# Performance work log

Measured on AMD Instinct MI355X. Metric: run time of the kernel, lower is better.

## Reference

```python
import jax, jax.numpy as jnp
import numpy as np

# static config (Phi-3-like with GQA)
B, S, H, HKV, D, BS = 2, 2048, 32, 8, 128, 64
HID = H * D
NB = B * (S // BS)  # total cache blocks
THETA = 10000.0


def rotate_half(x):
    x1, x2 = jnp.split(x, 2, axis=-1)
    return jnp.concatenate([-x2, x1], axis=-1)


def rope_cos_sin(positions):
    # positions: [T] int -> cos/sin [T, D]
    inv_freq = 1.0 / (THETA ** (jnp.arange(0, D, 2, dtype=jnp.float32) / D))
    freqs = positions.astype(jnp.float32)[:, None] * inv_freq[None, :]
    emb = jnp.concatenate([freqs, freqs], axis=-1)
    return jnp.cos(emb), jnp.sin(emb)


def setup_inputs() -> dict:
    key = jax.random.key(0)
    k1, k2, k3 = jax.random.split(key, 3)
    T = B * S
    hidden_states = jax.random.normal(k1, (T, HID), dtype=jnp.float32)
    w_qkv = jax.random.normal(k2, ((H + 2 * HKV) * D, HID), dtype=jnp.float32) * 0.02
    w_o = jax.random.normal(k3, (HID, H * D), dtype=jnp.float32) * 0.02
    k_cache = jnp.zeros((NB, BS, HKV, D), dtype=jnp.float32)
    v_cache = jnp.zeros((NB, BS, HKV, D), dtype=jnp.float32)
    position_ids = jnp.tile(jnp.arange(S, dtype=jnp.int32), B)  # per-token positions (prefill)
    block_offsets = jnp.arange(NB, dtype=jnp.int32).reshape(B, S // BS)
    return dict(hidden_states=hidden_states, w_qkv=w_qkv, w_o=w_o,
                k_cache=k_cache, v_cache=v_cache, position_ids=position_ids,
                block_offsets=block_offsets, window_size=1024)


def reference(hidden_states, w_qkv, w_o, k_cache, v_cache, position_ids, block_offsets, window_size):
    # fused qkv projection + split
    qkv = hidden_states @ w_qkv.T  # [T, (H+2*HKV)*D]
    q, k, v = jnp.split(qkv, [H * D, H * D + HKV * D], axis=-1)
    q = q.reshape(-1, H, D)
    k = k.reshape(-1, HKV, D)
    v = v.reshape(-1, HKV, D)

    # rotary embedding on flattened tokens
    cos, sin = rope_cos_sin(position_ids)  # [T, D]
    cos, sin = cos[:, None, :], sin[:, None, :]
    q = q * cos + rotate_half(q) * sin
    k = k * cos + rotate_half(k) * sin

    # fill paged KV cache: token t of seq b -> block block_offsets[b, t//BS], slot t%BS
    flat_blocks = block_offsets.reshape(-1)  # [NB]
    k_blk = k.reshape(NB, BS, HKV, D)
    v_blk = v.reshape(NB, BS, HKV, D)
    k_cache = k_cache.at[flat_blocks].set(k_blk)
    v_cache = v_cache.at[flat_blocks].set(v_blk)

    # paged attention: gather per-sequence K/V through the block table
    k_seq = k_cache[block_offsets].reshape(B, S, HKV, D)
    v_seq = v_cache[block_offsets].reshape(B, S, HKV, D)

    G = H // HKV  # query heads per kv head (GQA)
    qh = q.reshape(B, S, HKV, G, D)
    scale = 1.0 / jnp.sqrt(jnp.float32(D))
    scores = jnp.einsum('bshgd,bthd->bhgst', qh, k_seq) * scale  # [B,HKV,G,S,S]

    # causal + sliding-window mask: j <= i and i - j < window_size
    i = jnp.arange(S)[:, None]
    j = jnp.arange(S)[None, :]
    mask = (j <= i) & ((i - j) < window_size)  # [S,S]
    scores = jnp.where(mask[None, None, None], scores, jnp.finfo(scores.dtype).min)
    probs = jax.nn.softmax(scores, axis=-1)

    out = jnp.einsum('bhgst,bthd->bshgd', probs, v_seq)  # [B,S,HKV,G,D]
    out = out.reshape(B * S, H * D)
    return out @ w_o.T  # [T, HID]
```

## Files before the change

### kernel.cpp

```cpp
#include <hip/hip_runtime.h>
#include <hip/hip_bf16.h>
#include <stdint.h>

typedef unsigned short u16;
typedef __attribute__((ext_vector_type(8))) short short8;
typedef __attribute__((ext_vector_type(8))) unsigned short u16x8;
typedef __attribute__((ext_vector_type(4))) float f32x4;
typedef __attribute__((ext_vector_type(16))) float f32x16;

#define B_    2
#define S_    2048
#define H_    32
#define HKV_  8
#define D_    128
#define HID_  4096
#define QKVW_ 6144

__device__ __forceinline__ u16 f2bf(float f){
  uint32_t b = __builtin_bit_cast(uint32_t, f);
  b += 0x7FFFu + ((b >> 16) & 1u);
  return (u16)(b >> 16);
}
__device__ __forceinline__ float bf2f(u16 h){
  uint32_t b = ((uint32_t)h) << 16;
  return __builtin_bit_cast(float, b);
}
__device__ __forceinline__ u16 bfc(float f){
  __hip_bfloat16 h = __float2bfloat16(f);
  return __builtin_bit_cast(u16, h);
}
__device__ __forceinline__ uint32_t cvtpk(float a, float b){
  uint32_t r;
  asm("v_cvt_pk_bf16_f32 %0, %1, %2" : "=v"(r) : "v"(a), "v"(b));
  return r;
}
__device__ __forceinline__ void pl32swap(uint32_t &a, uint32_t &b){
  asm volatile("v_permlane32_swap_b32 %0, %1" : "+v"(a), "+v"(b));
}

__device__ __forceinline__ void gload16(const u16* g, u16* l){
  __builtin_amdgcn_global_load_lds((const __attribute__((address_space(1))) void*)g,
                                   (__attribute__((address_space(3))) void*)l, 16, 0, 0);
}

__global__ void cvt3_kernel(const float* __restrict__ a, const float* __restrict__ b,
                            const float* __restrict__ c, u16* __restrict__ da,
                            u16* __restrict__ db, u16* __restrict__ dc){
  const int n1 = HID_*HID_/4;
  const int n2 = n1 + QKVW_*HID_/4;
  const int n3 = n2 + HID_*HID_/4;
  int i = blockIdx.x * blockDim.x + threadIdx.x;
  int stride = gridDim.x * blockDim.x;
  for (; i < n3; i += stride){
    const float* s; u16* d; int j;
    if (i < n1){ s = a; d = da; j = i; }
    else if (i < n2){ s = b; d = db; j = i - n1; }
    else { s = c; d = dc; j = i - n2; }
    float4 v = reinterpret_cast<const float4*>(s)[j];
    union { u16 u[4]; unsigned long long ll; } o;
    o.u[0] = f2bf(v.x); o.u[1] = f2bf(v.y); o.u[2] = f2bf(v.z); o.u[3] = f2bf(v.w);
    reinterpret_cast<unsigned long long*>(d)[j] = o.ll;
  }
}

__global__ void rope_table_kernel(float2* __restrict__ tab){
  int idx = blockIdx.x * blockDim.x + threadIdx.x;
  if (idx >= S_ * 64) return;
  int pos = idx >> 6, p = idx & 63;
  float inv = powf(10000.0f, -(float)p / 64.0f);
  float ang = (float)pos * inv;
  tab[idx] = make_float2(cosf(ang), sinf(ang));
}

__global__ void rope_k_kernel(u16* __restrict__ qkv, const int* __restrict__ pos_ids,
                              const float2* __restrict__ tab){
  int t = blockIdx.x;
  int pos = pos_ids[t];
  const float2* tb = tab + pos * 64;
  u16* row = qkv + (size_t)t * QKVW_ + HID_;
  for (int it = threadIdx.x; it < HKV_ * 64; it += 256){
    int hh = it >> 6, p = it & 63;
    int base = hh * D_;
    float x1 = bf2f(row[base + p]);
    float x2 = bf2f(row[base + 64 + p]);
    float2 cs = tb[p];
    row[base + p]      = f2bf(x1 * cs.x - x2 * cs.y);
    row[base + 64 + p] = f2bf(x2 * cs.x + x1 * cs.y);
  }
}

#define MFMA_(a, b, c)   __builtin_amdgcn_mfma_f32_16x16x32_bf16((a), (b), (c), 0, 0, 0)
#define MFMA32_(a, b, c) __builtin_amdgcn_mfma_f32_32x32x16_bf16((a), (b), (c), 0, 0, 0)

__global__ __launch_bounds__(256) void gemm128(const u16* __restrict__ A, const u16* __restrict__ B,
                                               u16* __restrict__ C, int M, int N, int K){
  __shared__ u16 As[128*64];
  __shared__ u16 Bs[128*64];
  const int tid  = threadIdx.x;
  const int wave = tid >> 6, lane = tid & 63;
  const int hi = lane >> 4, lo = lane & 15;
  const int bn = blockIdx.x, bm = blockIdx.y;
  const int wm = (wave >> 1) * 64, wn = (wave & 1) * 64;
  f32x4 acc[4][4] = {};

  const u16* ap[4]; const u16* bp[4];
  u16* lA[4]; u16* lB[4];
  #pragma unroll
  for (int p = 0; p < 4; p++){
    int e   = p*2048 + wave*512 + lane*8;
    int row = e >> 6;
    int cs  = ((e >> 3) & 7) ^ (row & 7);
    ap[p] = A + (size_t)(bm*128 + row) * K + cs*8;
    bp[p] = B + (size_t)(bn*128 + row) * K + cs*8;
    lA[p] = &As[p*2048 + wave*512];
    lB[p] = &Bs[p*2048 + wave*512];
  }
  const int sw = lo & 7;
  const int nk = K >> 6;
  for (int t = 0; t < nk; t++){
    #pragma unroll
    for (int p = 0; p < 4; p++){
      gload16(ap[p], lA[p]);
      gload16(bp[p], lB[p]);
      ap[p] += 64; bp[p] += 64;
    }
    __syncthreads();
    #pragma unroll
    for (int kk = 0; kk < 2; kk++){
      short8 af[4], bf[4];
      int sz = ((kk*4 + hi) ^ sw) * 8;
      #pragma unroll
      for (int mt = 0; mt < 4; mt++) af[mt] = *(const short8*)&As[(wm + mt*16 + lo)*64 + sz];
      #pragma unroll
      for (int nt = 0; nt < 4; nt++) bf[nt] = *(const short8*)&Bs[(wn + nt*16 + lo)*64 + sz];
      #pragma unroll
      for (int mt = 0; mt < 4; mt++)
        #pragma unroll
        for (int nt = 0; nt < 4; nt++)
          acc[mt][nt] = MFMA_(af[mt], bf[nt], acc[mt][nt]);
    }
    __syncthreads();
  }
  #pragma unroll
  for (int mt = 0; mt < 4; mt++){
    int row = bm*128 + wm + mt*16 + 4*hi;
    #pragma unroll
    for (int nt = 0; nt < 4; nt++){
      int col = bn*128 + wn + nt*16 + lo;
      #pragma unroll
      for (int r = 0; r < 4; r++)
        C[(size_t)(row + r)*N + col] = f2bf(acc[mt][nt][r]);
    }
  }
}

__global__ __launch_bounds__(512, 2) void gemm256(const u16* __restrict__ A, const u16* __restrict__ B,
                                                  float* __restrict__ C, int M, int N, int K, int nbn){
  __shared__ u16 As[2][16384];
  __shared__ u16 Bs[2][16384];
  const int tid = threadIdx.x;
  const int wave = tid >> 6, lane = tid & 63, lo = lane & 15, hi = lane >> 4;
  const int wr = wave >> 2, wc = wave & 3;
  const int sw = lo & 7;

  const int nwg = gridDim.x, bid = blockIdx.x, cpx = nwg >> 3;
  const int wg = (bid & 7) * cpx + (bid >> 3);
  const int bm = wg / nbn, bn = wg - bm * nbn;

  f32x4 acc[8][4] = {};

  const int pr0 = tid >> 3;
  const int sc0 = (tid & 7) ^ (pr0 & 7);
  const u16* aS0 = A + ((size_t)(bm*256 + pr0      ))*K + sc0*8;
  const u16* aS1 = A + ((size_t)(bm*256 + pr0 + 128))*K + sc0*8;
  const u16* aS2 = A + ((size_t)(bm*256 + pr0 + 64 ))*K + sc0*8;
  const u16* aS3 = A + ((size_t)(bm*256 + pr0 + 192))*K + sc0*8;
  const u16* bS0 = B + ((size_t)(bn*256 + pr0      ))*K + sc0*8;
  const u16* bS1 = B + ((size_t)(bn*256 + pr0 + 64 ))*K + sc0*8;
  const u16* bS2 = B + ((size_t)(bn*256 + pr0 + 128))*K + sc0*8;
  const u16* bS3 = B + ((size_t)(bn*256 + pr0 + 192))*K + sc0*8;
  const int dOfs = tid * 8;

  gload16(bS0, &Bs[0][dOfs]);        gload16(bS1, &Bs[0][4096 + dOfs]);
  gload16(bS2, &Bs[0][8192 + dOfs]); gload16(bS3, &Bs[0][12288 + dOfs]);
  gload16(aS0, &As[0][dOfs]);        gload16(aS1, &As[0][4096 + dOfs]);
  gload16(aS2, &As[0][8192 + dOfs]); gload16(aS3, &As[0][12288 + dOfs]);
  asm volatile("s_waitcnt vmcnt(0)" ::: "memory");
  __builtin_amdgcn_s_barrier();

  const int nk = K >> 6;
  for (int t = 0; t < nk; ++t){
    const int cur = t & 1, nxt = cur ^ 1;
    const u16* Ac = &As[cur][0];
    const u16* Bc = &Bs[cur][0];
    u16* An = &As[nxt][0];
    u16* Bn = &Bs[nxt][0];
    const size_t ko = (size_t)(t + 1) * 64;
    const bool more = (t + 1 < nk);
    short8 avr[4], bvr[8];

    #define RD_A(q) \
      _Pragma("unroll") for (int mt = 0; mt < 2; mt++) \
        _Pragma("unroll") for (int kk = 0; kk < 2; kk++){ \
          int ra = wr*128 + (q)*32 + mt*16 + lo; \
          int fo = ((ra & 63) << 6) + ((ra & 64) ? 8192 : 0) + ((ra & 128) ? 4096 : 0) \
                 + ((((kk << 2) + hi) ^ sw) << 3); \
          avr[mt*2 + kk] = *(const short8*)&Ac[fo]; \
        }
    #define DO_MFMA(q) \
      __builtin_amdgcn_s_setprio(1); \
      _Pragma("unroll") for (int mt = 0; mt < 2; mt++) \
        _Pragma("unroll") for (int nt = 0; nt < 4; nt++) \
          _Pragma("unroll") for (int kk = 0; kk < 2; kk++) \
            acc[(q)*2 + mt][nt] = MFMA_(avr[mt*2 + kk], bvr[nt*2 + kk], acc[(q)*2 + mt][nt]); \
      __builtin_amdgcn_s_setprio(0);

    #pragma unroll
    for (int nt = 0; nt < 4; nt++)
      #pragma unroll
      for (int kk = 0; kk < 2; kk++){
        int rb = wc*64 + nt*16 + lo;
        int fo = (rb << 6) + ((((kk << 2) + hi) ^ sw) << 3);
        bvr[nt*2 + kk] = *(const short8*)&Bc[fo];
      }
    RD_A(0)
    if (more){ gload16(bS0 + ko, Bn + dOfs); gload16(bS1 + ko, Bn + 4096 + dOfs); }
    __builtin_amdgcn_s_barrier();
    DO_MFMA(0)
    __builtin_amdgcn_s_barrier();

    RD_A(1)
    if (more){
      gload16(bS2 + ko, Bn + 8192 + dOfs); gload16(bS3 + ko, Bn + 12288 + dOfs);
      asm volatile("s_waitcnt vmcnt(4)" ::: "memory");
    } else {
      asm volatile("s_waitcnt vmcnt(0)" ::: "memory");
    }
    __builtin_amdgcn_sched_barrier(0);
    __builtin_amdgcn_s_barrier();
    DO_MFMA(1)
    __builtin_amdgcn_s_barrier();

    RD_A(2)
    if (more){ gload16(aS0 + ko, An + dOfs); gload16(aS1 + ko, An + 4096 + dOfs); }
    __builtin_amdgcn_s_barrier();
    DO_MFMA(2)
    __builtin_amdgcn_s_barrier();

    RD_A(3)
    if (more){ gload16(aS2 + ko, An + 8192 + dOfs); gload16(aS3 + ko, An + 12288 + dOfs); }
    asm volatile("s_waitcnt vmcnt(2)" ::: "memory");
    __builtin_amdgcn_sched_barrier(0);
    __builtin_amdgcn_s_barrier();
    DO_MFMA(3)
    __builtin_amdgcn_s_barrier();
    #undef RD_A
    #undef DO_MFMA
  }

  #pragma unroll
  for (int mtg = 0; mtg < 8; mtg++){
    int row = bm*256 + wr*128 + mtg*16 + 4*hi;
    #pragma unroll
    for (int nt = 0; nt < 4; nt++){
      int col = bn*256 + wc*64 + nt*16 + lo;
      #pragma unroll
      for (int r = 0; r < 4; r++)
        C[(size_t)(row + r)*N + col] = acc[mtg][nt][r];
    }
  }
}

__global__ __launch_bounds__(256, 2) void attn_kernel(const u16* __restrict__ qkv, u16* __restrict__ out,
                                                      const int* __restrict__ winp,
                                                      const int* __restrict__ pos_ids,
                                                      const float2* __restrict__ tab){
  const int id = blockIdx.x;
  const int hkv = id & 7;
  const int qtr = (id >> 3) & 15;
  const int gb  = id >> 7;
  const int qt  = (qtr + 3*gb) & 15;
  const int g = gb & 3, b = gb >> 2;
  const int h = hkv*4 + g;
  const int q0 = qt * 128;
  const int tid = threadIdx.x, wave = tid >> 6, lane = tid & 63;
  const int ql = lane & 31, hl = lane >> 5;
  const int win = winp[0];

  __shared__ u16 Ks[2][64*128];
  __shared__ u16 VT[2][128*64];

  const int qw = q0 + wave*32;
  short8 qf[8];
  {
    const u16* qp = qkv + (size_t)(b*S_ + qw + ql)*QKVW_ + h*D_ + hl*8;
    #pragma unroll
    for (int c = 0; c < 8; c++) qf[c] = *(const short8*)(qp + c*16);
    const float QS = 0.08838834764831845f * 1.4426950408889634f;
    int pos = pos_ids[b*S_ + qw + ql];
    const float2* tb = tab + pos*64 + hl*8;
    #pragma unroll
    for (int c = 0; c < 4; c++)
      #pragma unroll
      for (int i = 0; i < 8; i++){
        float2 cs = tb[c*16 + i];
        float x1 = bf2f((u16)qf[c][i]), x2 = bf2f((u16)qf[c+4][i]);
        qf[c][i]   = (short)bfc((x1*cs.x - x2*cs.y) * QS);
        qf[c+4][i] = (short)bfc((x2*cs.x + x1*cs.y) * QS);
      }
  }

  f32x16 acc[4] = {};
  float m_r = -3.0e38f, l_r = 0.0f;

  int js = q0 - (win - 1); if (js < 0) js = 0; js &= ~63;
  const int nt = (q0 + 128 - js) >> 6;

  const u16* Kg = qkv + (size_t)HID_ + hkv*D_;
  const u16* Vg = qkv + (size_t)HID_ + HKV_*D_ + hkv*D_;
  const int jp = tid & 31, d0 = (tid >> 5) * 16;

  const u16* ksrc[4];
  #pragma unroll
  for (int p = 0; p < 4; p++){
    int e = p*256 + tid;
    int row = e >> 4;
    int ss = (e & 15) ^ (row & 15);
    ksrc[p] = Kg + (size_t)(b*S_ + js + row)*QKVW_ + ss*8;
  }
  const u16* vsrc = Vg + (size_t)(b*S_ + js + 2*jp)*QKVW_ + d0;

  u16x8 vr0, vr1, vr2, vr3;
  {
    #pragma unroll
    for (int p = 0; p < 4; p++) gload16(ksrc[p], &Ks[0][p*2048 + wave*512]);
    vr0 = *(const u16x8*)(vsrc);
    vr1 = *(const u16x8*)(vsrc + 8);
    vr2 = *(const u16x8*)(vsrc + QKVW_);
    vr3 = *(const u16x8*)(vsrc + QKVW_ + 8);
    uint32_t* VT32 = (uint32_t*)&VT[0][0];
    #pragma unroll
    for (int i = 0; i < 8; i++){
      int da = d0 + i, db = d0 + 8 + i;
      VT32[da*32 + (jp ^ ((da & 7) << 2))] = (uint32_t)vr0[i] | ((uint32_t)vr2[i] << 16);
      VT32[db*32 + (jp ^ ((db & 7) << 2))] = (uint32_t)vr1[i] | ((uint32_t)vr3[i] << 16);
    }
  }
  __syncthreads();

  for (int t = 0; t < nt; t++){
    const int jc = js + t*64;
    const int cur = t & 1, nxt = cur ^ 1;
    const bool more = (t + 1 < nt);
    if (more){
      const size_t adv = (size_t)(t+1) * 64 * QKVW_;
      #pragma unroll
      for (int p = 0; p < 4; p++) gload16(ksrc[p] + adv, &Ks[nxt][p*2048 + wave*512]);
      const u16* vp = vsrc + adv;
      vr0 = *(const u16x8*)(vp);
      vr1 = *(const u16x8*)(vp + 8);
      vr2 = *(const u16x8*)(vp + QKVW_);
      vr3 = *(const u16x8*)(vp + QKVW_ + 8);
    }
    if (jc <= qw + 31 && jc + 63 >= qw - win + 1){
      f32x16 s0 = {}, s1 = {};
      const int sl = ql & 15;
      __builtin_amdgcn_s_setprio(1);
      #pragma unroll
      for (int c = 0; c < 8; c++){
        int so = (((c*2 + hl) ^ sl) * 8);
        short8 k0 = *(const short8*)&Ks[cur][ql*128 + so];
        short8 k1 = *(const short8*)&Ks[cur][(32 + ql)*128 + so];
        s0 = MFMA32_(k0, qf[c], s0);
        s1 = MFMA32_(k1, qf[c], s1);
      }
      __builtin_amdgcn_s_setprio(0);
      const int qa = qw + ql;
      const bool fullv = (jc + 63 <= qw) && (jc >= qw + 32 - win);
      if (!fullv){
        #pragma unroll
        for (int r = 0; r < 16; r++){
          int j0 = jc + (r&3) + 8*(r>>2) + 4*hl;
          if (j0 > qa || qa - j0 >= win) s0[r] = -3.0e38f;
          int j1 = j0 + 32;
          if (j1 > qa || qa - j1 >= win) s1[r] = -3.0e38f;
        }
      }
      float mx = s0[0];
      #pragma unroll
      for (int r = 1; r < 16; r++) mx = fmaxf(mx, s0[r]);
      #pragma unroll
      for (int r = 0; r < 16; r++) mx = fmaxf(mx, s1[r]);
      mx = fmaxf(mx, __shfl_xor(mx, 32));
      if (__any(mx > m_r + 8.0f)){
        float mn = fmaxf(m_r, mx);
        float al = exp2f(m_r - mn);
        m_r = mn; l_r *= al;
        #pragma unroll
        for (int r = 0; r < 16; r++){
          float a = __shfl(al, (r&3) + 8*(r>>2) + 4*hl);
          acc[0][r] *= a; acc[1][r] *= a; acc[2][r] *= a; acc[3][r] *= a;
        }
      }
      float ps = 0.f;
      if (fullv){
        #pragma unroll
        for (int r = 0; r < 16; r++){
          s0[r] = exp2f(s0[r] - m_r); s1[r] = exp2f(s1[r] - m_r);
          ps += s0[r] + s1[r];
        }
      } else {
        #pragma unroll
        for (int r = 0; r < 16; r++){
          s0[r] = s0[r] > -1e37f ? exp2f(s0[r] - m_r) : 0.f;
          s1[r] = s1[r] > -1e37f ? exp2f(s1[r] - m_r) : 0.f;
          ps += s0[r] + s1[r];
        }
      }
      ps += __shfl_xor(ps, 32);
      l_r += ps;
      short8 pa[4];
      #define MKFRAG(dst, P, o) { \
        uint32_t x1 = cvtpk(P[o+0], P[o+1]), x2 = cvtpk(P[o+2], P[o+3]); \
        uint32_t y1 = cvtpk(P[o+4], P[o+5]), y2 = cvtpk(P[o+6], P[o+7]); \
        pl32swap(x1, y1); pl32swap(x2, y2); \
        union { uint32_t w[4]; short8 v; } u_; \
        u_.w[0] = x1; u_.w[1] = x2; u_.w[2] = y1; u_.w[3] = y2; \
        dst = u_.v; }
      MKFRAG(pa[0], s0, 0)
      MKFRAG(pa[1], s0, 8)
      MKFRAG(pa[2], s1, 0)
      MKFRAG(pa[3], s1, 8)
      #undef MKFRAG
      __builtin_amdgcn_s_setprio(1);
      #pragma unroll
      for (int dt = 0; dt < 4; dt++){
        const int dr = dt*32 + ql;
        const u16* vb = &VT[cur][dr*64];
        const int sb = dr & 7;
        #pragma unroll
        for (int ks = 0; ks < 4; ks++){
          short8 vf = *(const short8*)&vb[(((ks*2 + hl) ^ sb) * 8)];
          acc[dt] = MFMA32_(pa[ks], vf, acc[dt]);
        }
      }
      __builtin_amdgcn_s_setprio(0);
    }
    if (more){
      uint32_t* VT32 = (uint32_t*)&VT[nxt][0];
      #pragma unroll
      for (int i = 0; i < 8; i++){
        int da = d0 + i, db = d0 + 8 + i;
        VT32[da*32 + (jp ^ ((da & 7) << 2))] = (uint32_t)vr0[i] | ((uint32_t)vr2[i] << 16);
        VT32[db*32 + (jp ^ ((db & 7) << 2))] = (uint32_t)vr1[i] | ((uint32_t)vr3[i] << 16);
      }
      __syncthreads();
    }
  }
  #pragma unroll
  for (int r = 0; r < 16; r++){
    int qrow = (r&3) + 8*(r>>2) + 4*hl;
    float lr = __shfl(l_r, qrow);
    float invl = 1.0f / lr;
    size_t ro = (size_t)(b*S_ + qw + qrow)*HID_ + h*D_ + ql;
    out[ro     ] = f2bf(acc[0][r] * invl);
    out[ro + 32] = f2bf(acc[1][r] * invl);
    out[ro + 64] = f2bf(acc[2][r] * invl);
    out[ro + 96] = f2bf(acc[3][r] * invl);
  }
}

extern "C" void kernel_launch(void* const* d_in, const int* in_sizes, int n_in,
                              void* d_out, int out_size, void* d_ws, size_t ws_size,
                              hipStream_t stream) {
  const float* hs   = (const float*)d_in[0];
  const float* wqkv = (const float*)d_in[1];
  const float* wo   = (const float*)d_in[2];
  const int* pos  = (const int*)d_in[5];
  const int* winp = (const int*)d_in[7];
  float* out = (float*)d_out;

  u16* hsb = (u16*)d_ws;
  u16* wqb = hsb + (size_t)HID_*HID_;
  u16* wob = wqb + (size_t)QKVW_*HID_;
  u16* qkv = wob + (size_t)HID_*HID_;
  u16* att = qkv + (size_t)(B_*S_)*QKVW_;
  float2* tab = (float2*)(att + (size_t)(B_*S_)*HID_);

  cvt3_kernel<<<2048, 256, 0, stream>>>(hs, wqkv, wo, hsb, wqb, wob);
  rope_table_kernel<<<(S_*64 + 255)/256, 256, 0, stream>>>(tab);
  gemm128<<<dim3(QKVW_/128, (B_*S_)/128), 256, 0, stream>>>(hsb, wqb, qkv, B_*S_, QKVW_, HID_);
  rope_k_kernel<<<B_*S_, 256, 0, stream>>>(qkv, pos, tab);
  attn_kernel<<<1024, 256, 0, stream>>>(qkv, att, winp, pos, tab);
  gemm256<<<(B_*S_/256)*(HID_/256), 512, 0, stream>>>(att, wob, out, B_*S_, HID_, HID_, HID_/256);
}
```

Baseline: 522.3 us.

## Restructure output GEMM into quadrant-split 256x256 pipeline with split LDS halves

Replaces the output-projection GEMM with a templated variant that splits A and B tiles into 128-row halves in LDS and computes the 256x256 tile as four 128x128 quadrant MFMA phases. Each wave now holds a 4x2 subtile per quadrant, and the global prefetch of the next K step is interleaved with the quadrants so loads for stage t+2 are issued into freed halves while stage t computes. The aim is deeper load/compute overlap and more fragment reuse per LDS read. In exchange the barrier structure and vmcnt accounting become more intricate, and a bf16 output path is added through a template flag.

Measured after the change: 523.7 us. About the same (+0.3%).

```diff
diff --git a/kernel.cpp b/kernel.cpp
--- a/kernel.cpp
+++ b/kernel.cpp
@@ -154,121 +154,123 @@
   }
 }
 
-__global__ __launch_bounds__(512, 2) void gemm256(const u16* __restrict__ A, const u16* __restrict__ B,
-                                                  float* __restrict__ C, int M, int N, int K, int nbn){
-  __shared__ u16 As[2][16384];
-  __shared__ u16 Bs[2][16384];
+template<int CF>
+__global__ __launch_bounds__(512, 2) void gemm256p8(const u16* __restrict__ A, const u16* __restrict__ B,
+                                                    void* __restrict__ Cv, int M, int N, int K, int nbn){
+  __shared__ u16 As[2][2][8192];
+  __shared__ u16 Bs[2][2][8192];
   const int tid = threadIdx.x;
   const int wave = tid >> 6, lane = tid & 63, lo = lane & 15, hi = lane >> 4;
-  const int wr = wave >> 2, wc = wave & 3;
+  const int wr = (wave >> 2) & 1, wc = wave & 3;
   const int sw = lo & 7;
 
   const int nwg = gridDim.x, bid = blockIdx.x, cpx = nwg >> 3;
   const int wg = (bid & 7) * cpx + (bid >> 3);
   const int bm = wg / nbn, bn = wg - bm * nbn;
 
-  f32x4 acc[8][4] = {};
+  f32x4 acc[2][4][2][2] = {};
 
   const int pr0 = tid >> 3;
   const int sc0 = (tid & 7) ^ (pr0 & 7);
-  const u16* aS0 = A + ((size_t)(bm*256 + pr0      ))*K + sc0*8;
-  const u16* aS1 = A + ((size_t)(bm*256 + pr0 + 128))*K + sc0*8;
-  const u16* aS2 = A + ((size_t)(bm*256 + pr0 + 64 ))*K + sc0*8;
-  const u16* aS3 = A + ((size_t)(bm*256 + pr0 + 192))*K + sc0*8;
-  const u16* bS0 = B + ((size_t)(bn*256 + pr0      ))*K + sc0*8;
-  const u16* bS1 = B + ((size_t)(bn*256 + pr0 + 64 ))*K + sc0*8;
-  const u16* bS2 = B + ((size_t)(bn*256 + pr0 + 128))*K + sc0*8;
-  const u16* bS3 = B + ((size_t)(bn*256 + pr0 + 192))*K + sc0*8;
+  const u16* aSrc[2][2]; const u16* bSrc[2][2];
+  #pragma unroll
+  for (int h = 0; h < 2; h++)
+    #pragma unroll
+    for (int j = 0; j < 2; j++){
+      aSrc[h][j] = A + (size_t)(bm*256 + h*128 + j*64 + pr0)*K + sc0*8;
+      bSrc[h][j] = B + (size_t)(bn*256 + h*128 + j*64 + pr0)*K + sc0*8;
+    }
   const int dOfs = tid * 8;
 
-  gload16(bS0, &Bs[0][dOfs]);        gload16(bS1, &Bs[0][4096 + dOfs]);
-  gload16(bS2, &Bs[0][8192 + dOfs]); gload16(bS3, &Bs[0][12288 + dOfs]);
-  gload16(aS0, &As[0][dOfs]);        gload16(aS1, &As[0][4096 + dOfs]);
-  gload16(aS2, &As[0][8192 + dOfs]); gload16(aS3, &As[0][12288 + dOfs]);
-  asm volatile("s_waitcnt vmcnt(0)" ::: "memory");
+  #define STG_A(d, h, ko) { gload16(aSrc[h][0] + (ko), &As[d][h][dOfs]); \
+                            gload16(aSrc[h][1] + (ko), &As[d][h][4096 + dOfs]); }
+  #define STG_B(d, h, ko) { gload16(bSrc[h][0] + (ko), &Bs[d][h][dOfs]); \
+                            gload16(bSrc[h][1] + (ko), &Bs[d][h][4096 + dOfs]); }
+  #define RD_AF(d, q) \
+    _Pragma("unroll") for (int mt = 0; mt < 4; mt++) \
+      _Pragma("unroll") for (int kk = 0; kk < 2; kk++) \
+        af[mt*2+kk] = *(const short8*)&As[d][q][(wr*64 + mt*16 + lo)*64 + ((((kk<<2)+hi)^sw)<<3)];
+  #define RD_BF(dst, d, n) \
+    _Pragma("unroll") for (int nt = 0; nt < 2; nt++) \
+      _Pragma("unroll") for (int kk = 0; kk < 2; kk++) \
+        dst[nt*2+kk] = *(const short8*)&Bs[d][n][(wc*32 + nt*16 + lo)*64 + ((((kk<<2)+hi)^sw)<<3)];
+  #define DO_MFMA(q, n, bfv) \
+    __builtin_amdgcn_s_setprio(1); \
+    _Pragma("unroll") for (int mt = 0; mt < 4; mt++) \
+      _Pragma("unroll") for (int nt = 0; nt < 2; nt++) \
+        _Pragma("unroll") for (int kk = 0; kk < 2; kk++) \
+          acc[q][mt][n][nt] = MFMA_(af[mt*2+kk], bfv[nt*2+kk], acc[q][mt][n][nt]); \
+    __builtin_amdgcn_s_setprio(0);
+
+  const int nk = K >> 6;
+  STG_A(0, 0, 0) STG_B(0, 0, 0) STG_A(0, 1, 0) STG_B(0, 1, 0)
+  if (nk > 1){ STG_B(1, 0, 64) STG_A(1, 1, 64) STG_B(1, 1, 64)
+    asm volatile("s_waitcnt vmcnt(6)" ::: "memory");
+  } else {
+    asm volatile("s_waitcnt vmcnt(0)" ::: "memory");
+  }
   __builtin_amdgcn_s_barrier();
 
-  const int nk = K >> 6;
   for (int t = 0; t < nk; ++t){
-    const int cur = t & 1, nxt = cur ^ 1;
-    const u16* Ac = &As[cur][0];
-    const u16* Bc = &Bs[cur][0];
-    u16* An = &As[nxt][0];
-    u16* Bn = &Bs[nxt][0];
-    const size_t ko = (size_t)(t + 1) * 64;
-    const bool more = (t + 1 < nk);
-    short8 avr[4], bvr[8];
-
-    #define RD_A(q) \
-      _Pragma("unroll") for (int mt = 0; mt < 2; mt++) \
-        _Pragma("unroll") for (int kk = 0; kk < 2; kk++){ \
-          int ra = wr*128 + (q)*32 + mt*16 + lo; \
-          int fo = ((ra & 63) << 6) + ((ra & 64) ? 8192 : 0) + ((ra & 128) ? 4096 : 0) \
-                 + ((((kk << 2) + hi) ^ sw) << 3); \
-          avr[mt*2 + kk] = *(const short8*)&Ac[fo]; \
-        }
-    #define DO_MFMA(q) \
-      __builtin_amdgcn_s_setprio(1); \
-      _Pragma("unroll") for (int mt = 0; mt < 2; mt++) \
-        _Pragma("unroll") for (int nt = 0; nt < 4; nt++) \
-          _Pragma("unroll") for (int kk = 0; kk < 2; kk++) \
-            acc[(q)*2 + mt][nt] = MFMA_(avr[mt*2 + kk], bvr[nt*2 + kk], acc[(q)*2 + mt][nt]); \
-      __builtin_amdgcn_s_setprio(0);
-
-    #pragma unroll
-    for (int nt = 0; nt < 4; nt++)
-      #pragma unroll
-      for (int kk = 0; kk < 2; kk++){
-        int rb = wc*64 + nt*16 + lo;
-        int fo = (rb << 6) + ((((kk << 2) + hi) ^ sw) << 3);
-        bvr[nt*2 + kk] = *(const short8*)&Bc[fo];
-      }
-    RD_A(0)
-    if (more){ gload16(bS0 + ko, Bn + dOfs); gload16(bS1 + ko, Bn + 4096 + dOfs); }
-    __builtin_amdgcn_s_barrier();
-    DO_MFMA(0)
-    __builtin_amdgcn_s_barrier();
-
-    RD_A(1)
-    if (more){
-      gload16(bS2 + ko, Bn + 8192 + dOfs); gload16(bS3 + ko, Bn + 12288 + dOfs);
-      asm volatile("s_waitcnt vmcnt(4)" ::: "memory");
+    const int d = t & 1, dn = d ^ 1;
+    const size_t ko1 = (size_t)(t+1) * 64, ko2 = (size_t)(t+2) * 64;
+    const bool m1 = (t + 1 < nk), m2 = (t + 2 < nk);
+    short8 af[8], bf0[4], bf1[4];
+
+    RD_AF(d, 0)
+    RD_BF(bf0, d, 0)
+    if (m1){ STG_A(dn, 0, ko1) }
+    __builtin_amdgcn_s_barrier();
+    DO_MFMA(0, 0, bf0)
+    __builtin_amdgcn_s_barrier();
+
+    RD_AF(d, 1)
+    if (m2){ STG_B(d, 0, ko2) }
+    __builtin_amdgcn_s_barrier();
+    DO_MFMA(1, 0, bf0)
+    __builtin_amdgcn_s_barrier();
+
+    RD_BF(bf1, d, 1)
+    if (m2){ STG_A(d, 1, ko2) }
+    __builtin_amdgcn_s_barrier();
+    DO_MFMA(1, 1, bf1)
+    __builtin_amdgcn_s_barrier();
+
+    RD_AF(d, 0)
+    if (m2){
+      STG_B(d, 1, ko2)
+      asm volatile("s_waitcnt vmcnt(6)" ::: "memory");
     } else {
       asm volatile("s_waitcnt vmcnt(0)" ::: "memory");
     }
     __builtin_amdgcn_sched_barrier(0);
     __builtin_amdgcn_s_barrier();
-    DO_MFMA(1)
-    __builtin_amdgcn_s_barrier();
-
-    RD_A(2)
-    if (more){ gload16(aS0 + ko, An + dOfs); gload16(aS1 + ko, An + 4096 + dOfs); }
-    __builtin_amdgcn_s_barrier();
-    DO_MFMA(2)
-    __builtin_amdgcn_s_barrier();
-
-    RD_A(3)
-    if (more){ gload16(aS2 + ko, An + 8192 + dOfs); gload16(aS3 + ko, An + 12288 + dOfs); }
-    asm volatile("s_waitcnt vmcnt(2)" ::: "memory");
-    __builtin_amdgcn_sched_barrier(0);
-    __builtin_amdgcn_s_barrier();
-    DO_MFMA(3)
-    __builtin_amdgcn_s_barrier();
-    #undef RD_A
-    #undef DO_MFMA
-  }
-
-  #pragma unroll
-  for (int mtg = 0; mtg < 8; mtg++){
-    int row = bm*256 + wr*128 + mtg*16 + 4*hi;
-    #pragma unroll
-    for (int nt = 0; nt < 4; nt++){
-      int col = bn*256 + wc*64 + nt*16 + lo;
-      #pragma unroll
-      for (int r = 0; r < 4; r++)
-        C[(size_t)(row + r)*N + col] = acc[mtg][nt][r];
-    }
-  }
+    DO_MFMA(0, 1, bf1)
+    __builtin_amdgcn_s_barrier();
+  }
+  #undef STG_A
+  #undef STG_B
+  #undef RD_AF
+  #undef RD_BF
+  #undef DO_MFMA
+
+  #pragma unroll
+  for (int q = 0; q < 2; q++)
+    #pragma unroll
+    for (int mt = 0; mt < 4; mt++){
+      int row = bm*256 + q*128 + wr*64 + mt*16 + 4*hi;
+      #pragma unroll
+      for (int n = 0; n < 2; n++)
+        #pragma unroll
+        for (int nt = 0; nt < 2; nt++){
+          int col = bn*256 + n*128 + wc*32 + nt*16 + lo;
+          #pragma unroll
+          for (int r = 0; r < 4; r++){
+            if (CF == 0) ((u16*)Cv)[(size_t)(row + r)*N + col] = f2bf(acc[q][mt][n][nt][r]);
+            else         ((float*)Cv)[(size_t)(row + r)*N + col] = acc[q][mt][n][nt][r];
+          }
+        }
+    }
 }
 
 __global__ __launch_bounds__(256, 2) void attn_kernel(const u16* __restrict__ qkv, u16* __restrict__ out,
@@ -492,5 +494,5 @@
   gemm128<<<dim3(QKVW_/128, (B_*S_)/128), 256, 0, stream>>>(hsb, wqb, qkv, B_*S_, QKVW_, HID_);
   rope_k_kernel<<<B_*S_, 256, 0, stream>>>(qkv, pos, tab);
   attn_kernel<<<1024, 256, 0, stream>>>(qkv, att, winp, pos, tab);
-  gemm256<<<(B_*S_/256)*(HID_/256), 512, 0, stream>>>(att, wob, out, B_*S_, HID_, HID_, HID_/256);
-}
+  gemm256p8<1><<<(B_*S_/256)*(HID_/256), 512, 0, stream>>>(att, wob, (void*)out, B_*S_, HID_, HID_, HID_/256);
+}
```
